# Kernel tuning notes

Hardware: AMD Instinct MI355X
Metric: run time of the kernel (lower is better)

## Reference

```python
import jax, jax.numpy as jnp
import numpy as np

# Model config (matches init_kwargs)
E, TOP_K, H, I = 16, 2, 2048, 1024
B, S = 2, 2048
GROUP = 16                 # NVFP4 quantization group size along contraction dim
RSF = 1.0                  # routed_scaling_factor


def setup_inputs() -> dict:
    key = jax.random.key(0)
    ks = jax.random.split(key, 6)
    hidden_states = jax.random.normal(ks[0], (B, S, H), dtype=jnp.float32)
    gate_weight = jax.random.normal(ks[1], (E, H), dtype=jnp.float32) * 0.02
    # int4 codes stored as int32 in [0,16); reference subtracts 8 -> [-8,7]
    fc_up_qweights = jax.random.randint(ks[2], (E, H, I), 0, 16, dtype=jnp.int32)
    fc_up_blocks_scale = jax.random.uniform(ks[3], (E, H // GROUP, I), dtype=jnp.float32) * 0.02
    fc_up_global_scale = jnp.ones((1,), dtype=jnp.float32)
    fc_down_qweights = jax.random.randint(ks[4], (E, I, H), 0, 16, dtype=jnp.int32)
    fc_down_blocks_scale = jax.random.uniform(ks[5], (E, I // GROUP, H), dtype=jnp.float32) * 0.02
    fc_down_global_scale = jnp.ones((1,), dtype=jnp.float32)
    return {
        'hidden_states': hidden_states,
        'gate_weight': gate_weight,
        'fc_up_blocks_scale': fc_up_blocks_scale,
        'fc_up_global_scale': fc_up_global_scale,
        'fc_down_blocks_scale': fc_down_blocks_scale,
        'fc_down_global_scale': fc_down_global_scale,
        'fc_up_qweights': fc_up_qweights,
        'fc_down_qweights': fc_down_qweights,
    }


def _dequant(q, blocks_scale, global_scale):
    # q: [E,K,N] int codes (0..15 -> -8..7); blocks_scale: [E,K/GROUP,N]
    e, k, n = q.shape
    w = (q.astype(jnp.float32) - 8.0).reshape(e, k // GROUP, GROUP, n)
    w = w * blocks_scale[:, :, None, :]
    return w.reshape(e, k, n) * global_scale[0]


def reference(hidden_states, gate_weight, fc_up_blocks_scale, fc_up_global_scale,
              fc_down_blocks_scale, fc_down_global_scale,
              fc_up_qweights, fc_down_qweights):
    b, s, h = hidden_states.shape
    x = hidden_states.reshape(-1, h).astype(jnp.float32)          # [T,H]
    t = x.shape[0]

    # Router: HF sigmoid routing mapped through logsigmoid so that
    # softmax(logsigmoid(l)) == sigmoid(l)/sum(sigmoid(l))  (nemotron_h_plugin_router_logits)
    logits = jax.nn.log_sigmoid(x @ gate_weight.T)                # [T,E]
    probs = jax.nn.softmax(logits, axis=-1)
    topw, topi = jax.lax.top_k(probs, TOP_K)                      # [T,K]
    topw = topw / (jnp.sum(topw, axis=-1, keepdims=True) + 1e-20) # renormalize

    # Dense per-token expert weights [T,E] (scatter of top-k weights)
    wdense = jnp.zeros((t, E), dtype=jnp.float32)
    wdense = wdense.at[jnp.arange(t)[:, None], topi].add(topw) * RSF

    w_up = _dequant(fc_up_qweights, fc_up_blocks_scale, fc_up_global_scale)     # [E,H,I]
    w_down = _dequant(fc_down_qweights, fc_down_blocks_scale, fc_down_global_scale)  # [E,I,H]

    z = jnp.einsum('th,ehi->tei', x, w_up)                        # up proj
    a = jnp.square(jnp.maximum(z, 0.0))                           # activation_type=0: ReLU^2
    aw = a * wdense[:, :, None]                                   # fold routing weights (linear)
    y = jnp.einsum('tei,eih->th', aw, w_down)                     # down proj + combine
    return y.reshape(b, s, h)
```

## Files before the change

### kernel.cpp

```cpp
#include <hip/hip_runtime.h>

#define TOK 4096
#define NE 16
#define HD 2048
#define ID 1024
#define QGROUP 16
#define CAP 4096

typedef _Float16 half4v __attribute__((ext_vector_type(4)));
typedef _Float16 half8v __attribute__((ext_vector_type(8)));
typedef float float4v __attribute__((ext_vector_type(4)));

__device__ __forceinline__ void g2l16(const void* g, void* l) {
    __builtin_amdgcn_global_load_lds(
        (const __attribute__((address_space(1))) unsigned int*)g,
        (__attribute__((address_space(3))) unsigned int*)l, 16, 0, 0);
}

__global__ __launch_bounds__(256) void prep_kernel(
    const float* __restrict__ x, _Float16* __restrict__ xh)
{
    int i8 = (blockIdx.x * 256 + threadIdx.x) * 8;
    float4 f0 = *(const float4*)&x[i8];
    float4 f1 = *(const float4*)&x[i8 + 4];
    half8v h;
    h[0] = (_Float16)f0.x; h[1] = (_Float16)f0.y; h[2] = (_Float16)f0.z; h[3] = (_Float16)f0.w;
    h[4] = (_Float16)f1.x; h[5] = (_Float16)f1.y; h[6] = (_Float16)f1.z; h[7] = (_Float16)f1.w;
    *(half8v*)&xh[i8] = h;
}

__global__ __launch_bounds__(256) void router_kernel(
    const float* __restrict__ x, const float* __restrict__ gw,
    int* __restrict__ topi, float* __restrict__ topw)
{
    int t = blockIdx.x;
    int tid = threadIdx.x;
    float p[NE];
#pragma unroll
    for (int e = 0; e < NE; e++) p[e] = 0.f;
    const float* xr = x + (size_t)t * HD;
    for (int h = tid; h < HD; h += 256) {
        float xv = xr[h];
#pragma unroll
        for (int e = 0; e < NE; e++) p[e] = fmaf(xv, gw[e * HD + h], p[e]);
    }
#pragma unroll
    for (int off = 32; off > 0; off >>= 1) {
#pragma unroll
        for (int e = 0; e < NE; e++) p[e] += __shfl_down(p[e], off, 64);
    }
    __shared__ float part[4][NE];
    int wave = tid >> 6, lane = tid & 63;
    if (lane == 0) {
#pragma unroll
        for (int e = 0; e < NE; e++) part[wave][e] = p[e];
    }
    __syncthreads();
    if (tid == 0) {
        float s[NE]; float sum = 0.f;
#pragma unroll
        for (int e = 0; e < NE; e++) {
            float l = part[0][e] + part[1][e] + part[2][e] + part[3][e];
            float sg = 1.f / (1.f + expf(-l));
            s[e] = sg; sum += sg;
        }
        int i1 = 0;
#pragma unroll
        for (int e = 1; e < NE; e++) if (s[e] > s[i1]) i1 = e;
        int i2 = (i1 == 0) ? 1 : 0;
#pragma unroll
        for (int e = 0; e < NE; e++) if (e != i1 && s[e] > s[i2]) i2 = e;
        float p1 = s[i1] / sum, p2 = s[i2] / sum;
        float inv = 1.f / (p1 + p2 + 1e-20f);
        topi[t * 2 + 0] = i1; topw[t * 2 + 0] = p1 * inv;
        topi[t * 2 + 1] = i2; topw[t * 2 + 1] = p2 * inv;
    }
}

__global__ __launch_bounds__(256) void compact_kernel(
    const int* __restrict__ topi, const float* __restrict__ topw,
    int* __restrict__ counts, int* __restrict__ pair_row, float* __restrict__ pair_w)
{
    const int e = blockIdx.x;
    const int tid = threadIdx.x;
    const int lane = tid & 63, wv = tid >> 6;
    __shared__ int wsum[4];
    int running = 0;
    for (int base = 0; base < 2 * TOK; base += 256) {
        const int idx = base + tid;
        const bool f = (topi[idx] == e);
        unsigned long long b = __ballot(f);
        int pre = __popcll(b & ((1ull << lane) - 1ull));
        if (lane == 0) wsum[wv] = __popcll(b);
        __syncthreads();
        int woff = 0;
#pragma unroll
        for (int w = 0; w < 4; w++) if (w < wv) woff += wsum[w];
        const int tot = wsum[0] + wsum[1] + wsum[2] + wsum[3];
        if (f) {
            const int pos = running + woff + pre;
            pair_row[e * CAP + pos] = idx;
            pair_w[e * CAP + pos] = topw[idx];
        }
        running += tot;
        __syncthreads();
    }
    if (tid == 0) counts[e] = running;
}

template<int K, int N>
__global__ __launch_bounds__(256) void dequantT_kernel(
    const int* __restrict__ qw, const float* __restrict__ bsc, _Float16* __restrict__ wq)
{
    const int e = blockIdx.z, kt = blockIdx.y, nt = blockIdx.x;
    const int tid = threadIdx.x;
    __shared__ _Float16 T[64][68];

    const int c4 = (tid & 15) * 4;
    const int r0 = tid >> 4;
#pragma unroll
    for (int p = 0; p < 4; p++) {
        const int r = p * 16 + r0;
        const int kabs = kt * 64 + r;
        const int4 c = *(const int4*)&qw[((size_t)e * K + kabs) * N + nt * 64 + c4];
        const float4 sc = *(const float4*)&bsc[((size_t)e * (K / QGROUP) + (kabs >> 4)) * N + nt * 64 + c4];
        half4v h;
        h[0] = (_Float16)((float)(c.x - 8) * sc.x);
        h[1] = (_Float16)((float)(c.y - 8) * sc.y);
        h[2] = (_Float16)((float)(c.z - 8) * sc.z);
        h[3] = (_Float16)((float)(c.w - 8) * sc.w);
        *(half4v*)&T[r][c4] = h;
    }
    __syncthreads();
    const int nrow = tid >> 2;
    const int kseg = (tid & 3) * 16;
    half8v o0, o1;
#pragma unroll
    for (int i = 0; i < 8; i++) o0[i] = T[kseg + i][nrow];
#pragma unroll
    for (int i = 0; i < 8; i++) o1[i] = T[kseg + 8 + i][nrow];
    _Float16* dst = wq + ((size_t)e * N + nt * 64 + nrow) * K + kt * 64 + kseg;
    *(half8v*)dst = o0;
    *(half8v*)(dst + 8) = o1;
}

template<int N, int K, bool UP>
__global__ __launch_bounds__(256, 5) void gemm5_kernel(
    const _Float16* __restrict__ A, const _Float16* __restrict__ BT,
    const float* __restrict__ gsc,
    const int* __restrict__ counts, const int* __restrict__ pair_row,
    const float* __restrict__ pair_w,
    _Float16* __restrict__ store16, float* __restrict__ store32)
{
    constexpr int NT = N / 128;
    constexpr int MT = CAP / 64;
    const int bx = blockIdx.x;
    const int g8 = bx & 7;
    const int rest = bx >> 3;
    const int m = rest % MT;
    const int g = (rest / MT) * 8 + g8;
    const int e = g / NT, nt = g % NT;
    const int cnt = counts[e];
    const int mbase = m * 64;
    if (mbase >= cnt) return;
    const int nbase = nt * 128;
    const int tid = threadIdx.x;

    __shared__ _Float16 As[64 * 64];
    __shared__ _Float16 Bs[128 * 64];
    __shared__ int rows_s[64];
    __shared__ float pw_s[64];

    if (tid < 64) {
        int idx = mbase + tid; if (idx >= cnt) idx = cnt - 1;
        rows_s[tid] = pair_row[e * CAP + idx];
        pw_s[tid] = UP ? pair_w[e * CAP + idx] : 0.f;
    }
    __syncthreads();

    const _Float16* asrc[2]; _Float16* adst[2];
#pragma unroll
    for (int j = 0; j < 2; j++) {
        const int gidx = j * 256 + tid;
        const int r = gidx >> 3, s = gidx & 7, c = s ^ (r & 7);
        const int pr = rows_s[r];
        asrc[j] = A + (size_t)(UP ? (pr >> 1) : pr) * K + c * 8;
        adst[j] = &As[r * 64 + s * 8];
    }
    const _Float16* bsrc[4]; _Float16* bdst[4];
#pragma unroll
    for (int j = 0; j < 4; j++) {
        const int gidx = j * 256 + tid;
        const int r = gidx >> 3, s = gidx & 7, c = s ^ (r & 7);
        bsrc[j] = BT + ((size_t)e * N + nbase + r) * K + c * 8;
        bdst[j] = &Bs[r * 64 + s * 8];
    }

    const int lane = tid & 63, wv = tid >> 6;
    const int quad = lane >> 4, lm = lane & 15;
    const int wm = (wv & 1) * 32, wn = (wv >> 1) * 64;

    float4v acc[2][4];
#pragma unroll
    for (int mi = 0; mi < 2; mi++)
#pragma unroll
        for (int ni = 0; ni < 4; ni++) acc[mi][ni] = (float4v){0.f, 0.f, 0.f, 0.f};

    for (int k0 = 0; k0 < K; k0 += 64) {
#pragma unroll
        for (int j = 0; j < 2; j++) g2l16(asrc[j] + k0, adst[j]);
#pragma unroll
        for (int j = 0; j < 4; j++) g2l16(bsrc[j] + k0, bdst[j]);
        __syncthreads();
#pragma unroll
        for (int ks = 0; ks < 2; ks++) {
            half8v af[2], bf[4];
#pragma unroll
            for (int mi = 0; mi < 2; mi++) {
                const int r = wm + mi * 16 + lm;
                const int s = (ks * 4 + quad) ^ (r & 7);
                af[mi] = *(const half8v*)&As[r * 64 + s * 8];
            }
#pragma unroll
            for (int ni = 0; ni < 4; ni++) {
                const int r = wn + ni * 16 + lm;
                const int s = (ks * 4 + quad) ^ (r & 7);
                bf[ni] = *(const half8v*)&Bs[r * 64 + s * 8];
            }
#pragma unroll
            for (int mi = 0; mi < 2; mi++)
#pragma unroll
                for (int ni = 0; ni < 4; ni++)
                    acc[mi][ni] = __builtin_amdgcn_mfma_f32_16x16x32_f16(af[mi], bf[ni], acc[mi][ni], 0, 0, 0);
        }
        __syncthreads();
    }

    const float gs = gsc[0];
#pragma unroll
    for (int mi = 0; mi < 2; mi++) {
#pragma unroll
        for (int r = 0; r < 4; r++) {
            const int rl = wm + mi * 16 + quad * 4 + r;
            if (mbase + rl < cnt) {
                const int pr = rows_s[rl];
#pragma unroll
                for (int ni = 0; ni < 4; ni++) {
                    const int col = nbase + wn + ni * 16 + lm;
                    float v = acc[mi][ni][r] * gs;
                    if (UP) {
                        v = fmaxf(v, 0.f);
                        v = v * v * pw_s[rl];
                        store16[(size_t)pr * N + col] = (_Float16)v;
                    } else {
                        atomicAdd(&store32[(size_t)(pr >> 1) * N + col], v);
                    }
                }
            }
        }
    }
}

template<int N, int K, bool UP>
__global__ __launch_bounds__(256) void gemm_fused_kernel(
    const _Float16* __restrict__ A, const int* __restrict__ qw,
    const float* __restrict__ bsc, const float* __restrict__ gsc,
    const int* __restrict__ counts, const int* __restrict__ pair_row,
    const float* __restrict__ pair_w,
    _Float16* __restrict__ store16, float* __restrict__ store32)
{
    constexpr int NT = N / 128;
    const int e = blockIdx.y;
    const int cnt = counts[e];
    const int mt = blockIdx.x / NT, nt = blockIdx.x % NT;
    const int mbase = mt * 128;
    if (mbase >= cnt) return;
    const int nbase = nt * 128;
    const int tid = threadIdx.x;

    __shared__ _Float16 As[128][40];
    __shared__ _Float16 Bs[128][40];
    __shared__ int rows_s[128];
    __shared__ float pw_s[128];

    if (tid < 128) {
        int idx = mbase + tid; if (idx >= cnt) idx = cnt - 1;
        rows_s[tid] = pair_row[e * CAP + idx];
        pw_s[tid] = UP ? pair_w[e * CAP + idx] : 0.f;
    }

    const int lane = tid & 63, wv = tid >> 6;
    const int quad = lane >> 4, lm = lane & 15;
    const int wr = (wv >> 1) * 64, wc = (wv & 1) * 64;

    float4v acc[4][4];
#pragma unroll
    for (int mi = 0; mi < 4; mi++)
#pragma unroll
        for (int ni = 0; ni < 4; ni++) acc[mi][ni] = (float4v){0.f, 0.f, 0.f, 0.f};

    const int am = tid & 127, akk = (tid >> 7) * 16;
    const int bn4 = (tid & 31) * 4, bkb = (tid >> 5) * 4;

    for (int k0 = 0; k0 < K; k0 += 32) {
        __syncthreads();
        {
            int pr = rows_s[am];
            const _Float16* src = A + (size_t)(UP ? (pr >> 1) : pr) * K + k0 + akk;
            *(uint4*)&As[am][akk] = *(const uint4*)src;
            *(uint4*)&As[am][akk + 8] = *(const uint4*)(src + 8);
        }
        {
            const int kabs = k0 + bkb;
            const float4 sc = *(const float4*)&bsc[((size_t)e * (K / QGROUP) + (kabs >> 4)) * N + nbase + bn4];
            const int4 c0 = *(const int4*)&qw[((size_t)e * K + kabs + 0) * N + nbase + bn4];
            const int4 c1 = *(const int4*)&qw[((size_t)e * K + kabs + 1) * N + nbase + bn4];
            const int4 c2 = *(const int4*)&qw[((size_t)e * K + kabs + 2) * N + nbase + bn4];
            const int4 c3 = *(const int4*)&qw[((size_t)e * K + kabs + 3) * N + nbase + bn4];
            half4v q;
            q[0] = (_Float16)((c0.x - 8) * sc.x); q[1] = (_Float16)((c1.x - 8) * sc.x);
            q[2] = (_Float16)((c2.x - 8) * sc.x); q[3] = (_Float16)((c3.x - 8) * sc.x);
            *(half4v*)&Bs[bn4 + 0][bkb] = q;
            q[0] = (_Float16)((c0.y - 8) * sc.y); q[1] = (_Float16)((c1.y - 8) * sc.y);
            q[2] = (_Float16)((c2.y - 8) * sc.y); q[3] = (_Float16)((c3.y - 8) * sc.y);
            *(half4v*)&Bs[bn4 + 1][bkb] = q;
            q[0] = (_Float16)((c0.z - 8) * sc.z); q[1] = (_Float16)((c1.z - 8) * sc.z);
            q[2] = (_Float16)((c2.z - 8) * sc.z); q[3] = (_Float16)((c3.z - 8) * sc.z);
            *(half4v*)&Bs[bn4 + 2][bkb] = q;
            q[0] = (_Float16)((c0.w - 8) * sc.w); q[1] = (_Float16)((c1.w - 8) * sc.w);
            q[2] = (_Float16)((c2.w - 8) * sc.w); q[3] = (_Float16)((c3.w - 8) * sc.w);
            *(half4v*)&Bs[bn4 + 3][bkb] = q;
        }
        __syncthreads();
        half8v af[4], bf[4];
#pragma unroll
        for (int mi = 0; mi < 4; mi++)
            af[mi] = *(const half8v*)&As[wr + mi * 16 + lm][quad * 8];
#pragma unroll
        for (int ni = 0; ni < 4; ni++)
            bf[ni] = *(const half8v*)&Bs[wc + ni * 16 + lm][quad * 8];
#pragma unroll
        for (int mi = 0; mi < 4; mi++)
#pragma unroll
            for (int ni = 0; ni < 4; ni++)
                acc[mi][ni] = __builtin_amdgcn_mfma_f32_16x16x32_f16(af[mi], bf[ni], acc[mi][ni], 0, 0, 0);
    }

    const float gs = gsc[0];
#pragma unroll
    for (int mi = 0; mi < 4; mi++) {
#pragma unroll
        for (int r = 0; r < 4; r++) {
            const int rl = wr + mi * 16 + quad * 4 + r;
            if (mbase + rl < cnt) {
                const int pr = rows_s[rl];
#pragma unroll
                for (int ni = 0; ni < 4; ni++) {
                    const int col = nbase + wc + ni * 16 + lm;
                    float v = acc[mi][ni][r] * gs;
                    if (UP) {
                        v = fmaxf(v, 0.f);
                        v = v * v * pw_s[rl];
                        store16[(size_t)pr * N + col] = (_Float16)v;
                    } else {
                        atomicAdd(&store32[(size_t)(pr >> 1) * N + col], v);
                    }
                }
            }
        }
    }
}

extern "C" void kernel_launch(void* const* d_in, const int* in_sizes, int n_in,
                              void* d_out, int out_size, void* d_ws, size_t ws_size,
                              hipStream_t stream) {
    const float* x   = (const float*)d_in[0];
    const float* gw  = (const float*)d_in[1];
    const float* usc = (const float*)d_in[2];
    const float* ugs = (const float*)d_in[3];
    const float* dsc = (const float*)d_in[4];
    const float* dgs = (const float*)d_in[5];
    const int*   uq  = (const int*)d_in[6];
    const int*   dq  = (const int*)d_in[7];
    float* out = (float*)d_out;

    char* ws = (char*)d_ws;
    int*   counts   = (int*)(ws + 0);
    int*   pair_row = (int*)(ws + 4096);
    float* pair_w   = (float*)(ws + 4096 + (size_t)NE * CAP * 4);
    _Float16* xh    = (_Float16*)(ws + 528384);
    _Float16* act   = (_Float16*)(ws + 528384 + (size_t)TOK * HD * 2);
    _Float16* wq    = (_Float16*)(ws + 528384 + (size_t)TOK * HD * 2
                                  + (size_t)2 * TOK * ID * 2);
    int*   topi = (int*)wq;
    float* topw = (float*)((char*)wq + (size_t)2 * TOK * 4);
    const size_t need_deq = 34082816ull + (size_t)NE * HD * ID * 2;
    const bool use_deq = ws_size >= need_deq;

    hipMemsetAsync(out, 0, (size_t)TOK * HD * 4, stream);

    prep_kernel<<<(TOK * HD) / (256 * 8), 256, 0, stream>>>(x, xh);
    router_kernel<<<TOK, 256, 0, stream>>>(x, gw, topi, topw);
    compact_kernel<<<NE, 256, 0, stream>>>(topi, topw, counts, pair_row, pair_w);

    if (use_deq) {
        dequantT_kernel<HD, ID><<<dim3(ID / 64, HD / 64, NE), 256, 0, stream>>>(uq, usc, wq);
        gemm5_kernel<ID, HD, true><<<(CAP / 64) * (ID / 128) * NE, 256, 0, stream>>>(
            xh, wq, ugs, counts, pair_row, pair_w, act, nullptr);
        dequantT_kernel<ID, HD><<<dim3(HD / 64, ID / 64, NE), 256, 0, stream>>>(dq, dsc, wq);
        gemm5_kernel<HD, ID, false><<<(CAP / 64) * (HD / 128) * NE, 256, 0, stream>>>(
            act, wq, dgs, counts, pair_row, pair_w, nullptr, out);
    } else {
        gemm_fused_kernel<ID, HD, true><<<dim3((CAP / 128) * (ID / 128), NE), 256, 0, stream>>>(
            xh, uq, usc, ugs, counts, pair_row, pair_w, act, nullptr);
        gemm_fused_kernel<HD, ID, false><<<dim3((CAP / 128) * (HD / 128), NE), 256, 0, stream>>>(
            act, dq, dsc, dgs, counts, pair_row, pair_w, nullptr, out);
    }
}
```

Before: 543.6 us.

## Double-buffer GEMM tiles, fuse fp16 cast into router, replace atomics with combine

The fp32-to-fp16 conversion of activations moves into the router kernel, and the router reads gate weights as float4. The grouped GEMM gets double-buffered LDS, so the next K tile's global-to-LDS loads overlap with the MFMA work on the current tile. Occupancy drops from 5 to 3 blocks because LDS use doubles. When workspace allows, the down projection writes per-pair fp16 partials instead of using fp32 atomics, and a combine kernel sums the two top-k contributions. This removes the output memset and the atomic traffic, but rounds the down-projection partials to fp16 before summation.

```diff
diff --git a/kernel.cpp b/kernel.cpp
--- a/kernel.cpp
+++ b/kernel.cpp
@@ -17,32 +17,28 @@
         (__attribute__((address_space(3))) unsigned int*)l, 16, 0, 0);
 }
 
-__global__ __launch_bounds__(256) void prep_kernel(
-    const float* __restrict__ x, _Float16* __restrict__ xh)
-{
-    int i8 = (blockIdx.x * 256 + threadIdx.x) * 8;
-    float4 f0 = *(const float4*)&x[i8];
-    float4 f1 = *(const float4*)&x[i8 + 4];
-    half8v h;
-    h[0] = (_Float16)f0.x; h[1] = (_Float16)f0.y; h[2] = (_Float16)f0.z; h[3] = (_Float16)f0.w;
-    h[4] = (_Float16)f1.x; h[5] = (_Float16)f1.y; h[6] = (_Float16)f1.z; h[7] = (_Float16)f1.w;
-    *(half8v*)&xh[i8] = h;
-}
-
 __global__ __launch_bounds__(256) void router_kernel(
     const float* __restrict__ x, const float* __restrict__ gw,
-    int* __restrict__ topi, float* __restrict__ topw)
-{
-    int t = blockIdx.x;
-    int tid = threadIdx.x;
+    _Float16* __restrict__ xh, int* __restrict__ topi, float* __restrict__ topw)
+{
+    const int t = blockIdx.x;
+    const int tid = threadIdx.x;
+    const int h8 = tid * 8;
+    const float* xr = x + (size_t)t * HD;
+    const float4 f0 = *(const float4*)&xr[h8];
+    const float4 f1 = *(const float4*)&xr[h8 + 4];
+    half8v hv;
+    hv[0] = (_Float16)f0.x; hv[1] = (_Float16)f0.y; hv[2] = (_Float16)f0.z; hv[3] = (_Float16)f0.w;
+    hv[4] = (_Float16)f1.x; hv[5] = (_Float16)f1.y; hv[6] = (_Float16)f1.z; hv[7] = (_Float16)f1.w;
+    *(half8v*)&xh[(size_t)t * HD + h8] = hv;
+
     float p[NE];
 #pragma unroll
-    for (int e = 0; e < NE; e++) p[e] = 0.f;
-    const float* xr = x + (size_t)t * HD;
-    for (int h = tid; h < HD; h += 256) {
-        float xv = xr[h];
-#pragma unroll
-        for (int e = 0; e < NE; e++) p[e] = fmaf(xv, gw[e * HD + h], p[e]);
+    for (int e = 0; e < NE; e++) {
+        const float4 g0 = *(const float4*)&gw[e * HD + h8];
+        const float4 g1 = *(const float4*)&gw[e * HD + h8 + 4];
+        p[e] = f0.x * g0.x + f0.y * g0.y + f0.z * g0.z + f0.w * g0.w
+             + f1.x * g1.x + f1.y * g1.y + f1.z * g1.z + f1.w * g1.w;
     }
 #pragma unroll
     for (int off = 32; off > 0; off >>= 1) {
@@ -145,7 +141,7 @@
 }
 
 template<int N, int K, bool UP>
-__global__ __launch_bounds__(256, 5) void gemm5_kernel(
+__global__ __launch_bounds__(256, 3) void gemm5_kernel(
     const _Float16* __restrict__ A, const _Float16* __restrict__ BT,
     const float* __restrict__ gsc,
     const int* __restrict__ counts, const int* __restrict__ pair_row,
@@ -166,8 +162,8 @@
     const int nbase = nt * 128;
     const int tid = threadIdx.x;
 
-    __shared__ _Float16 As[64 * 64];
-    __shared__ _Float16 Bs[128 * 64];
+    __shared__ _Float16 As[2][64 * 64];
+    __shared__ _Float16 Bs[2][128 * 64];
     __shared__ int rows_s[64];
     __shared__ float pw_s[64];
 
@@ -178,22 +174,22 @@
     }
     __syncthreads();
 
-    const _Float16* asrc[2]; _Float16* adst[2];
+    const _Float16* asrc[2]; int aoff[2];
 #pragma unroll
     for (int j = 0; j < 2; j++) {
         const int gidx = j * 256 + tid;
         const int r = gidx >> 3, s = gidx & 7, c = s ^ (r & 7);
         const int pr = rows_s[r];
         asrc[j] = A + (size_t)(UP ? (pr >> 1) : pr) * K + c * 8;
-        adst[j] = &As[r * 64 + s * 8];
-    }
-    const _Float16* bsrc[4]; _Float16* bdst[4];
+        aoff[j] = r * 64 + s * 8;
+    }
+    const _Float16* bsrc[4]; int boff[4];
 #pragma unroll
     for (int j = 0; j < 4; j++) {
         const int gidx = j * 256 + tid;
         const int r = gidx >> 3, s = gidx & 7, c = s ^ (r & 7);
         bsrc[j] = BT + ((size_t)e * N + nbase + r) * K + c * 8;
-        bdst[j] = &Bs[r * 64 + s * 8];
+        boff[j] = r * 64 + s * 8;
     }
 
     const int lane = tid & 63, wv = tid >> 6;
@@ -206,12 +202,21 @@
 #pragma unroll
         for (int ni = 0; ni < 4; ni++) acc[mi][ni] = (float4v){0.f, 0.f, 0.f, 0.f};
 
+#pragma unroll
+    for (int j = 0; j < 2; j++) g2l16(asrc[j], &As[0][aoff[j]]);
+#pragma unroll
+    for (int j = 0; j < 4; j++) g2l16(bsrc[j], &Bs[0][boff[j]]);
+    asm volatile("s_waitcnt vmcnt(0)" ::: "memory");
+    __builtin_amdgcn_s_barrier();
+
+    int cur = 0;
     for (int k0 = 0; k0 < K; k0 += 64) {
-#pragma unroll
-        for (int j = 0; j < 2; j++) g2l16(asrc[j] + k0, adst[j]);
-#pragma unroll
-        for (int j = 0; j < 4; j++) g2l16(bsrc[j] + k0, bdst[j]);
-        __syncthreads();
+        if (k0 + 64 < K) {
+#pragma unroll
+            for (int j = 0; j < 2; j++) g2l16(asrc[j] + k0 + 64, &As[cur ^ 1][aoff[j]]);
+#pragma unroll
+            for (int j = 0; j < 4; j++) g2l16(bsrc[j] + k0 + 64, &Bs[cur ^ 1][boff[j]]);
+        }
 #pragma unroll
         for (int ks = 0; ks < 2; ks++) {
             half8v af[2], bf[4];
@@ -219,13 +224,13 @@
             for (int mi = 0; mi < 2; mi++) {
                 const int r = wm + mi * 16 + lm;
                 const int s = (ks * 4 + quad) ^ (r & 7);
-                af[mi] = *(const half8v*)&As[r * 64 + s * 8];
+                af[mi] = *(const half8v*)&As[cur][r * 64 + s * 8];
             }
 #pragma unroll
             for (int ni = 0; ni < 4; ni++) {
                 const int r = wn + ni * 16 + lm;
                 const int s = (ks * 4 + quad) ^ (r & 7);
-                bf[ni] = *(const half8v*)&Bs[r * 64 + s * 8];
+                bf[ni] = *(const half8v*)&Bs[cur][r * 64 + s * 8];
             }
 #pragma unroll
             for (int mi = 0; mi < 2; mi++)
@@ -233,7 +238,9 @@
                 for (int ni = 0; ni < 4; ni++)
                     acc[mi][ni] = __builtin_amdgcn_mfma_f32_16x16x32_f16(af[mi], bf[ni], acc[mi][ni], 0, 0, 0);
         }
-        __syncthreads();
+        asm volatile("s_waitcnt vmcnt(0)" ::: "memory");
+        __builtin_amdgcn_s_barrier();
+        cur ^= 1;
     }
 
     const float gs = gsc[0];
@@ -252,6 +259,8 @@
                         v = fmaxf(v, 0.f);
                         v = v * v * pw_s[rl];
                         store16[(size_t)pr * N + col] = (_Float16)v;
+                    } else if (store16) {
+                        store16[(size_t)pr * N + col] = (_Float16)v;
                     } else {
                         atomicAdd(&store32[(size_t)(pr >> 1) * N + col], v);
                     }
@@ -259,6 +268,27 @@
             }
         }
     }
+}
+
+__global__ __launch_bounds__(256) void combine_kernel(
+    const _Float16* __restrict__ part, float* __restrict__ out)
+{
+    const size_t i8 = ((size_t)blockIdx.x * 256 + threadIdx.x) * 8;
+    const size_t t = i8 >> 11;
+    const int h = (int)(i8 & (HD - 1));
+    const half8v a = *(const half8v*)&part[(t * 2) * HD + h];
+    const half8v b = *(const half8v*)&part[(t * 2 + 1) * HD + h];
+    float4 o0, o1;
+    o0.x = (float)a[0] + (float)b[0];
+    o0.y = (float)a[1] + (float)b[1];
+    o0.z = (float)a[2] + (float)b[2];
+    o0.w = (float)a[3] + (float)b[3];
+    o1.x = (float)a[4] + (float)b[4];
+    o1.y = (float)a[5] + (float)b[5];
+    o1.z = (float)a[6] + (float)b[6];
+    o1.w = (float)a[7] + (float)b[7];
+    *(float4*)&out[i8] = o0;
+    *(float4*)&out[i8 + 4] = o1;
 }
 
 template<int N, int K, bool UP>
@@ -394,13 +424,15 @@
                                   + (size_t)2 * TOK * ID * 2);
     int*   topi = (int*)wq;
     float* topw = (float*)((char*)wq + (size_t)2 * TOK * 4);
-    const size_t need_deq = 34082816ull + (size_t)NE * HD * ID * 2;
-    const bool use_deq = ws_size >= need_deq;
-
-    hipMemsetAsync(out, 0, (size_t)TOK * HD * 4, stream);
-
-    prep_kernel<<<(TOK * HD) / (256 * 8), 256, 0, stream>>>(x, xh);
-    router_kernel<<<TOK, 256, 0, stream>>>(x, gw, topi, topw);
+    const size_t deq_end = 34082816ull + (size_t)NE * HD * ID * 2;
+    const bool use_deq = ws_size >= deq_end;
+    _Float16* part = (_Float16*)(ws + deq_end);
+    const bool use_part = use_deq && (ws_size >= deq_end + (size_t)2 * TOK * HD * 2);
+
+    if (!use_part)
+        hipMemsetAsync(out, 0, (size_t)TOK * HD * 4, stream);
+
+    router_kernel<<<TOK, 256, 0, stream>>>(x, gw, xh, topi, topw);
     compact_kernel<<<NE, 256, 0, stream>>>(topi, topw, counts, pair_row, pair_w);
 
     if (use_deq) {
@@ -409,7 +441,9 @@
             xh, wq, ugs, counts, pair_row, pair_w, act, nullptr);
         dequantT_kernel<ID, HD><<<dim3(HD / 64, ID / 64, NE), 256, 0, stream>>>(dq, dsc, wq);
         gemm5_kernel<HD, ID, false><<<(CAP / 64) * (HD / 128) * NE, 256, 0, stream>>>(
-            act, wq, dgs, counts, pair_row, pair_w, nullptr, out);
+            act, wq, dgs, counts, pair_row, pair_w, use_part ? part : nullptr, out);
+        if (use_part)
+            combine_kernel<<<(TOK * HD) / (256 * 8), 256, 0, stream>>>(part, out);
     } else {
         gemm_fused_kernel<ID, HD, true><<<dim3((CAP / 128) * (ID / 128), NE), 256, 0, stream>>>(
             xh, uq, usc, ugs, counts, pair_row, pair_w, act, nullptr);
```

After: 535.8 us. No clear change (-1.4%).
